# Optimization experiments

Measured on AMD Instinct MI355X. Metric: run time of the kernel, lower is better.

The kernel has to match this reference:

```python
import jax, jax.numpy as jnp
import numpy as np

N = 131072          # collocation points per dataset
C_WAVE = 1.0        # wave speed c
DIMS = [2, 256, 256, 256, 256, 1]


def _glorot(k, shape):
    fan_in, fan_out = shape
    std = jnp.sqrt(2.0 / (fan_in + fan_out)).astype(jnp.float32)
    return std * jax.random.normal(k, shape, dtype=jnp.float32)


def setup_inputs() -> dict:
    key = jax.random.key(0)
    ks = jax.random.split(key, 16)
    inp = {}
    for i in range(5):
        inp[f"W{i}"] = _glorot(ks[i], (DIMS[i], DIMS[i + 1]))
        inp[f"b{i}"] = jnp.zeros((DIMS[i + 1],), jnp.float32)
    inp["tx_equation"] = jax.random.uniform(ks[10], (N, 2), dtype=jnp.float32)
    inp["tx_init"] = jax.random.uniform(ks[11], (N, 2), dtype=jnp.float32)
    # initial condition points have t=0 in practice; values don't affect the math pattern
    inp["tx_init"] = inp["tx_init"].at[:, 0].set(0.0)
    inp["tx_bound"] = jax.random.uniform(ks[12], (N, 2), dtype=jnp.float32)
    return inp


def _mlp(params, tx):
    # tanh MLP: (..., 2) -> (..., 1)
    h = tx
    for W, b in params[:-1]:
        h = jnp.tanh(h @ W + b)
    W, b = params[-1]
    return h @ W + b


def reference(W0, b0, W1, b1, W2, b2, W3, b3, W4, b4,
              tx_equation, tx_init, tx_bound):
    params = [(W0, b0), (W1, b1), (W2, b2), (W3, b3), (W4, b4)]

    def u_scalar(tx):  # tx: (2,) -> scalar u(t, x)
        return _mlp(params, tx[None, :])[0, 0]

    # PDE residual: u_tt - c^2 * u_xx via per-point Hessian diagonal (input_diagonal_hessian)
    hess = jax.vmap(jax.hessian(u_scalar))(tx_equation)      # (N, 2, 2)
    u_tt = hess[:, 0, 0]
    u_xx = hess[:, 1, 1]
    pde_residual = (u_tt - (C_WAVE ** 2) * u_xx)[:, None]     # (N, 1)

    # Initial conditions: u and du/dt (input_gradient)
    u_init, g = jax.vmap(jax.value_and_grad(u_scalar))(tx_init)  # (N,), (N, 2)
    u_phi = u_init[:, None]                                   # (N, 1)
    du_dt_psi = g[:, 0][:, None]                              # (N, 1)

    # Boundary: plain forward
    u_bound = _mlp(params, tx_bound)                          # (N, 1)

    return jnp.stack([pde_residual, u_phi, du_dt_psi, u_bound], axis=0)  # (4, N, 1)
```

## Files before the change

kernel.cpp:

```cpp
#include <hip/hip_runtime.h>
#include <math.h>

#define N_PTS 131072
#define HID   256

typedef __attribute__((ext_vector_type(8)))  _Float16 f16x8;
typedef __attribute__((ext_vector_type(4)))  float    f32x4;
typedef __attribute__((ext_vector_type(16))) float    f32x16;
typedef unsigned int u32;
typedef __attribute__((address_space(1))) const u32 gu32;
typedef __attribute__((address_space(3))) u32       lu32;

#define LDS_ACT 0
#define LDS_B   32768
#define LDS_SZ  49152

__device__ __forceinline__ int act_addr(int row, int kbyte) {
    return row * 512 + ((kbyte + ((row & 31) << 4)) & 511);
}
__device__ __forceinline__ void tanh_f1(float z, float& h, float& f1) {
    float s = __expf(2.0f * z);
    float r = __builtin_amdgcn_rcpf(s + 1.0f);
    h  = fmaf(-2.0f, r, 1.0f);
    f1 = (1.0f - h) * (1.0f + h);
}

__global__ void prep_w(const float* __restrict__ W1, const float* __restrict__ W2,
                       const float* __restrict__ W3, char* __restrict__ ws)
{
    int idx = blockIdx.x * 256 + threadIdx.x;
    int l = idx >> 16;
    int e = idx & 65535;
    int k = e >> 8, n = e & 255;
    const float* W = (l == 0) ? W1 : (l == 1) ? W2 : W3;
    float w = W[e];
    int kc = k >> 4, hh = (k >> 3) & 1, kl = k & 7;
    int wq = n >> 5, nn = n & 31;
    size_t base = (size_t)((l * 16 + kc) * 8 + wq) * 1024;
    int byte_in = hh * 512 + nn * 16 + kl * 2;
    *(_Float16*)(ws + base + byte_in) = (_Float16)w;
}

template<int S, int PTS>
__global__ void __launch_bounds__(512, 4)
pinn_mfma(const float* __restrict__ W0, const float* __restrict__ b0,
          const float* __restrict__ b1, const float* __restrict__ b2,
          const float* __restrict__ b3,
          const float* __restrict__ W4, const float* __restrict__ b4,
          const char* __restrict__ wpre,
          const float* __restrict__ tx, float* __restrict__ out)
{
    extern __shared__ char lds[];
    const int tid  = threadIdx.x;
    const int lane = tid & 63;
    const int wid  = tid >> 6;
    const int l31  = lane & 31;
    const int hh   = lane >> 5;
    const int h16  = hh << 4;
    const int pbase = blockIdx.x * PTS;
    constexpr int CG = 512 / PTS;
    constexpr int NC = 256 / CG;
    const int ep  = tid / CG;
    const int ec0 = (tid % CG) * NC;

    {
        const float tt = tx[2 * (pbase + ep) + 0];
        const float xx = tx[2 * (pbase + ep) + 1];
        for (int cb = ec0; cb < ec0 + NC; cb += 8) {
            alignas(16) float w0r[8], w1r[8], bb[8];
            *(f32x4*)&w0r[0] = *(const f32x4*)(W0 + cb);
            *(f32x4*)&w0r[4] = *(const f32x4*)(W0 + cb + 4);
            *(f32x4*)&w1r[0] = *(const f32x4*)(W0 + HID + cb);
            *(f32x4*)&w1r[4] = *(const f32x4*)(W0 + HID + cb + 4);
            *(f32x4*)&bb[0]  = *(const f32x4*)(b0 + cb);
            *(f32x4*)&bb[4]  = *(const f32x4*)(b0 + cb + 4);
            f16x8 vhi[S];
            #pragma unroll
            for (int j = 0; j < 8; ++j) {
                float z = fmaf(tt, w0r[j], fmaf(xx, w1r[j], bb[j]));
                float h, f1;
                tanh_f1(z, h, f1);
                vhi[0][j] = (_Float16)h;
                if (S == 2) {
                    vhi[1][j] = (_Float16)(f1 * w0r[j]);
                } else if (S == 4) {
                    float d1 = w0r[j] + w1r[j];
                    float d2 = w0r[j] - w1r[j];
                    float f2 = -2.0f * h * f1;
                    vhi[1][j] = (_Float16)(f1 * d1);
                    vhi[2][j] = (_Float16)(f1 * d2);
                    vhi[3][j] = (_Float16)(f2 * d1 * d2);
                }
            }
            #pragma unroll
            for (int s2 = 0; s2 < S; ++s2) {
                int row = ep * S + s2;
                *(f16x8*)(lds + LDS_ACT + act_addr(row, cb * 2)) = vhi[s2];
            }
        }
    }

    const int c0 = wid * 32 + l31;
    const float b1a = b1[c0];
    const float b2a = b2[c0];
    const float b3a = b3[c0];

    const char* srcW = wpre + (size_t)wid * 1024 + lane * 16;
    char* dstW = lds + LDS_B + wid * 2048 + lane * 16;

    __builtin_amdgcn_sched_barrier(0);
    __builtin_amdgcn_global_load_lds((gu32*)srcW, (lu32*)dstW, 16, 0, 0);
    asm volatile("s_waitcnt lgkmcnt(0)" ::: "memory");
    __builtin_amdgcn_sched_barrier(0);
    __builtin_amdgcn_s_barrier();
    __builtin_amdgcn_sched_barrier(0);

    for (int l = 0; l < 3; ++l) {
        const float bias = (l == 0) ? b1a : (l == 1) ? b2a : b3a;
        const char* srcL = srcW + (size_t)l * 131072;

        f32x16 acc0 = (f32x16){0.f,0.f,0.f,0.f,0.f,0.f,0.f,0.f,
                               0.f,0.f,0.f,0.f,0.f,0.f,0.f,0.f};
        f32x16 acc1 = acc0;

        #pragma unroll
        for (int ph = 0; ph < 16; ++ph) {
            asm volatile("s_waitcnt vmcnt(0)" ::: "memory");

            const char* bslab = lds + LDS_B + wid * 2048 + (ph & 1) * 1024 + hh * 512;
            const int kbyte = ph * 32 + h16;
            f16x8 av0 = *(const f16x8*)(lds + LDS_ACT + act_addr(l31,      kbyte));
            f16x8 av1 = *(const f16x8*)(lds + LDS_ACT + act_addr(32 + l31, kbyte));
            f16x8 bv  = *(const f16x8*)(bslab + l31 * 16);

            if (ph < 15 || l < 2) {
                __builtin_amdgcn_global_load_lds(
                    (gu32*)(srcL + (size_t)(ph + 1) * 8192),
                    (lu32*)(dstW + ((ph + 1) & 1) * 1024), 16, 0, 0);
            }

            __builtin_amdgcn_s_setprio(1);
            acc0 = __builtin_amdgcn_mfma_f32_32x32x16_f16(av0, bv, acc0, 0, 0, 0);
            acc1 = __builtin_amdgcn_mfma_f32_32x32x16_f16(av1, bv, acc1, 0, 0, 0);
            __builtin_amdgcn_s_setprio(0);
        }
        __builtin_amdgcn_s_barrier();

        const bool lastL = (l == 2);
        const int colj = wid * 32 + l31;
        #pragma unroll
        for (int i = 0; i < 2; ++i) {
            const f32x16& A = i ? acc1 : acc0;
            const int rtb = i * 32 + 4 * hh;
            #pragma unroll
            for (int q = 0; q < 4; ++q) {
                const int rb = rtb + 8 * q;
                if (S == 4) {
                    float z0 = A[4*q+0] + bias;
                    float z1 = A[4*q+1];
                    float z2 = A[4*q+2];
                    float zm = A[4*q+3];
                    float h, f1;
                    tanh_f1(z0, h, f1);
                    float f2 = -2.0f * h * f1;
                    if (!lastL) {
                        *(_Float16*)(lds + LDS_ACT + act_addr(rb+0, colj*2)) = (_Float16)h;
                        *(_Float16*)(lds + LDS_ACT + act_addr(rb+1, colj*2)) = (_Float16)(f1 * z1);
                        *(_Float16*)(lds + LDS_ACT + act_addr(rb+2, colj*2)) = (_Float16)(f1 * z2);
                    }
                    *(_Float16*)(lds + LDS_ACT + act_addr(rb+3, colj*2)) =
                        (_Float16)(fmaf(f1, zm, f2 * z1 * z2));
                } else if (S == 2) {
                    #pragma unroll
                    for (int pp = 0; pp < 2; ++pp) {
                        float z0 = A[4*q+2*pp+0] + bias;
                        float zd = A[4*q+2*pp+1];
                        float h, f1;
                        tanh_f1(z0, h, f1);
                        *(_Float16*)(lds + LDS_ACT + act_addr(rb+2*pp+0, colj*2)) = (_Float16)h;
                        *(_Float16*)(lds + LDS_ACT + act_addr(rb+2*pp+1, colj*2)) = (_Float16)(f1 * zd);
                    }
                } else {
                    #pragma unroll
                    for (int m = 0; m < 4; ++m) {
                        float z0 = A[4*q+m] + bias;
                        float h, f1;
                        tanh_f1(z0, h, f1);
                        *(_Float16*)(lds + LDS_ACT + act_addr(rb+m, colj*2)) = (_Float16)h;
                    }
                }
            }
        }
        asm volatile("s_waitcnt lgkmcnt(0)" ::: "memory");
        __builtin_amdgcn_sched_barrier(0);
        __builtin_amdgcn_s_barrier();
        __builtin_amdgcn_sched_barrier(0);
    }

    if (S == 4) {
        const int p   = tid >> 5;
        const int seg = tid & 31;
        const int k0  = seg * 8;
        const int row = 4 * p + 3;
        f16x8 h8 = *(const f16x8*)(lds + LDS_ACT + act_addr(row, k0 * 2));
        alignas(16) float wv[8];
        *(f32x4*)&wv[0] = *(const f32x4*)(W4 + k0);
        *(f32x4*)&wv[4] = *(const f32x4*)(W4 + k0 + 4);
        float d = 0.0f;
        #pragma unroll
        for (int j = 0; j < 8; ++j) d = fmaf((float)h8[j], wv[j], d);
        #pragma unroll
        for (int off = 16; off > 0; off >>= 1) d += __shfl_down(d, off, 32);
        if (seg == 0) out[0 * N_PTS + pbase + p] = d;
    } else {
        const int row = tid >> 3;
        const int seg = tid & 7;
        const int k0  = seg * 32;
        float d = 0.0f;
        #pragma unroll
        for (int kb = 0; kb < 32; kb += 8) {
            f16x8 h8 = *(const f16x8*)(lds + LDS_ACT + act_addr(row, (k0 + kb) * 2));
            alignas(16) float wv[8];
            *(f32x4*)&wv[0] = *(const f32x4*)(W4 + k0 + kb);
            *(f32x4*)&wv[4] = *(const f32x4*)(W4 + k0 + kb + 4);
            #pragma unroll
            for (int j = 0; j < 8; ++j) d = fmaf((float)h8[j], wv[j], d);
        }
        d += __shfl_down(d, 4, 8);
        d += __shfl_down(d, 2, 8);
        d += __shfl_down(d, 1, 8);
        if (seg == 0) {
            if (S == 2) {
                const int p = row >> 1;
                if ((row & 1) == 0) out[1 * N_PTS + pbase + p] = d + b4[0];
                else                out[2 * N_PTS + pbase + p] = d;
            } else {
                out[3 * N_PTS + pbase + row] = d + b4[0];
            }
        }
    }
}

extern "C" void kernel_launch(void* const* d_in, const int* in_sizes, int n_in,
                              void* d_out, int out_size, void* d_ws, size_t ws_size,
                              hipStream_t stream) {
    const float* W0 = (const float*)d_in[0];
    const float* b0 = (const float*)d_in[1];
    const float* W1 = (const float*)d_in[2];
    const float* b1 = (const float*)d_in[3];
    const float* W2 = (const float*)d_in[4];
    const float* b2 = (const float*)d_in[5];
    const float* W3 = (const float*)d_in[6];
    const float* b3 = (const float*)d_in[7];
    const float* W4 = (const float*)d_in[8];
    const float* b4 = (const float*)d_in[9];
    const float* tx_eq    = (const float*)d_in[10];
    const float* tx_init  = (const float*)d_in[11];
    const float* tx_bound = (const float*)d_in[12];
    float* out = (float*)d_out;
    char* wpre = (char*)d_ws;

    prep_w<<<768, 256, 0, stream>>>(W1, W2, W3, wpre);
    pinn_mfma<4,16><<<N_PTS/16, 512, LDS_SZ, stream>>>(W0,b0,b1,b2,b3,W4,b4,wpre,tx_eq,   out);
    pinn_mfma<2,32><<<N_PTS/32, 512, LDS_SZ, stream>>>(W0,b0,b1,b2,b3,W4,b4,wpre,tx_init, out);
    pinn_mfma<1,64><<<N_PTS/64, 512, LDS_SZ, stream>>>(W0,b0,b1,b2,b3,W4,b4,wpre,tx_bound,out);
}
```

Baseline: 578.8 us.

## Hold MLP weight fragments in registers instead of staging through LDS

Weight B-fragments for each hidden layer are now loaded from global memory into a 16-entry register array and fed straight to the MFMAs. The next layer's fragments are prefetched into the same registers right after each MFMA pair. The LDS double-buffer and its per-phase vmcnt waits are removed, and LDS shrinks to a static 32 KB activation buffer. The aim is fewer LDS reads and waits in the inner loop and a smaller LDS footprint, at the cost of 64 extra VGPRs per thread under the existing launch bounds of 512 threads and 4 blocks.

```diff
diff --git a/kernel.cpp b/kernel.cpp
--- a/kernel.cpp
+++ b/kernel.cpp
@@ -7,13 +7,6 @@
 typedef __attribute__((ext_vector_type(8)))  _Float16 f16x8;
 typedef __attribute__((ext_vector_type(4)))  float    f32x4;
 typedef __attribute__((ext_vector_type(16))) float    f32x16;
-typedef unsigned int u32;
-typedef __attribute__((address_space(1))) const u32 gu32;
-typedef __attribute__((address_space(3))) u32       lu32;
-
-#define LDS_ACT 0
-#define LDS_B   32768
-#define LDS_SZ  49152
 
 __device__ __forceinline__ int act_addr(int row, int kbyte) {
     return row * 512 + ((kbyte + ((row & 31) << 4)) & 511);
@@ -50,7 +43,7 @@
           const char* __restrict__ wpre,
           const float* __restrict__ tx, float* __restrict__ out)
 {
-    extern __shared__ char lds[];
+    __shared__ char act[32768];
     const int tid  = threadIdx.x;
     const int lane = tid & 63;
     const int wid  = tid >> 6;
@@ -62,6 +55,13 @@
     constexpr int NC = 256 / CG;
     const int ep  = tid / CG;
     const int ec0 = (tid % CG) * NC;
+
+    const char* srcW = wpre + (size_t)wid * 1024 + lane * 16;
+
+    f16x8 bw[16];
+    #pragma unroll
+    for (int ph = 0; ph < 16; ++ph)
+        bw[ph] = *(const f16x8*)(srcW + (size_t)ph * 8192);
 
     {
         const float tt = tx[2 * (pbase + ep) + 0];
@@ -95,7 +95,7 @@
             #pragma unroll
             for (int s2 = 0; s2 < S; ++s2) {
                 int row = ep * S + s2;
-                *(f16x8*)(lds + LDS_ACT + act_addr(row, cb * 2)) = vhi[s2];
+                *(f16x8*)(act + act_addr(row, cb * 2)) = vhi[s2];
             }
         }
     }
@@ -105,11 +105,6 @@
     const float b2a = b2[c0];
     const float b3a = b3[c0];
 
-    const char* srcW = wpre + (size_t)wid * 1024 + lane * 16;
-    char* dstW = lds + LDS_B + wid * 2048 + lane * 16;
-
-    __builtin_amdgcn_sched_barrier(0);
-    __builtin_amdgcn_global_load_lds((gu32*)srcW, (lu32*)dstW, 16, 0, 0);
     asm volatile("s_waitcnt lgkmcnt(0)" ::: "memory");
     __builtin_amdgcn_sched_barrier(0);
     __builtin_amdgcn_s_barrier();
@@ -117,7 +112,8 @@
 
     for (int l = 0; l < 3; ++l) {
         const float bias = (l == 0) ? b1a : (l == 1) ? b2a : b3a;
-        const char* srcL = srcW + (size_t)l * 131072;
+        const char* srcNext = srcW + (size_t)(l + 1) * 131072;
+        const bool reload = (l < 2);
 
         f32x16 acc0 = (f32x16){0.f,0.f,0.f,0.f,0.f,0.f,0.f,0.f,
                                0.f,0.f,0.f,0.f,0.f,0.f,0.f,0.f};
@@ -125,24 +121,17 @@
 
         #pragma unroll
         for (int ph = 0; ph < 16; ++ph) {
-            asm volatile("s_waitcnt vmcnt(0)" ::: "memory");
-
-            const char* bslab = lds + LDS_B + wid * 2048 + (ph & 1) * 1024 + hh * 512;
             const int kbyte = ph * 32 + h16;
-            f16x8 av0 = *(const f16x8*)(lds + LDS_ACT + act_addr(l31,      kbyte));
-            f16x8 av1 = *(const f16x8*)(lds + LDS_ACT + act_addr(32 + l31, kbyte));
-            f16x8 bv  = *(const f16x8*)(bslab + l31 * 16);
-
-            if (ph < 15 || l < 2) {
-                __builtin_amdgcn_global_load_lds(
-                    (gu32*)(srcL + (size_t)(ph + 1) * 8192),
-                    (lu32*)(dstW + ((ph + 1) & 1) * 1024), 16, 0, 0);
-            }
+            f16x8 av0 = *(const f16x8*)(act + act_addr(l31,      kbyte));
+            f16x8 av1 = *(const f16x8*)(act + act_addr(32 + l31, kbyte));
 
             __builtin_amdgcn_s_setprio(1);
-            acc0 = __builtin_amdgcn_mfma_f32_32x32x16_f16(av0, bv, acc0, 0, 0, 0);
-            acc1 = __builtin_amdgcn_mfma_f32_32x32x16_f16(av1, bv, acc1, 0, 0, 0);
+            acc0 = __builtin_amdgcn_mfma_f32_32x32x16_f16(av0, bw[ph], acc0, 0, 0, 0);
+            acc1 = __builtin_amdgcn_mfma_f32_32x32x16_f16(av1, bw[ph], acc1, 0, 0, 0);
             __builtin_amdgcn_s_setprio(0);
+
+            if (reload)
+                bw[ph] = *(const f16x8*)(srcNext + (size_t)ph * 8192);
         }
         __builtin_amdgcn_s_barrier();
 
@@ -164,11 +153,11 @@
                     tanh_f1(z0, h, f1);
                     float f2 = -2.0f * h * f1;
                     if (!lastL) {
-                        *(_Float16*)(lds + LDS_ACT + act_addr(rb+0, colj*2)) = (_Float16)h;
-                        *(_Float16*)(lds + LDS_ACT + act_addr(rb+1, colj*2)) = (_Float16)(f1 * z1);
-                        *(_Float16*)(lds + LDS_ACT + act_addr(rb+2, colj*2)) = (_Float16)(f1 * z2);
+                        *(_Float16*)(act + act_addr(rb+0, colj*2)) = (_Float16)h;
+                        *(_Float16*)(act + act_addr(rb+1, colj*2)) = (_Float16)(f1 * z1);
+                        *(_Float16*)(act + act_addr(rb+2, colj*2)) = (_Float16)(f1 * z2);
                     }
-                    *(_Float16*)(lds + LDS_ACT + act_addr(rb+3, colj*2)) =
+                    *(_Float16*)(act + act_addr(rb+3, colj*2)) =
                         (_Float16)(fmaf(f1, zm, f2 * z1 * z2));
                 } else if (S == 2) {
                     #pragma unroll
@@ -177,8 +166,8 @@
                         float zd = A[4*q+2*pp+1];
                         float h, f1;
                         tanh_f1(z0, h, f1);
-                        *(_Float16*)(lds + LDS_ACT + act_addr(rb+2*pp+0, colj*2)) = (_Float16)h;
-                        *(_Float16*)(lds + LDS_ACT + act_addr(rb+2*pp+1, colj*2)) = (_Float16)(f1 * zd);
+                        *(_Float16*)(act + act_addr(rb+2*pp+0, colj*2)) = (_Float16)h;
+                        *(_Float16*)(act + act_addr(rb+2*pp+1, colj*2)) = (_Float16)(f1 * zd);
                     }
                 } else {
                     #pragma unroll
@@ -186,7 +175,7 @@
                         float z0 = A[4*q+m] + bias;
                         float h, f1;
                         tanh_f1(z0, h, f1);
-                        *(_Float16*)(lds + LDS_ACT + act_addr(rb+m, colj*2)) = (_Float16)h;
+                        *(_Float16*)(act + act_addr(rb+m, colj*2)) = (_Float16)h;
                     }
                 }
             }
@@ -202,7 +191,7 @@
         const int seg = tid & 31;
         const int k0  = seg * 8;
         const int row = 4 * p + 3;
-        f16x8 h8 = *(const f16x8*)(lds + LDS_ACT + act_addr(row, k0 * 2));
+        f16x8 h8 = *(const f16x8*)(act + act_addr(row, k0 * 2));
         alignas(16) float wv[8];
         *(f32x4*)&wv[0] = *(const f32x4*)(W4 + k0);
         *(f32x4*)&wv[4] = *(const f32x4*)(W4 + k0 + 4);
@@ -219,7 +208,7 @@
         float d = 0.0f;
         #pragma unroll
         for (int kb = 0; kb < 32; kb += 8) {
-            f16x8 h8 = *(const f16x8*)(lds + LDS_ACT + act_addr(row, (k0 + kb) * 2));
+            f16x8 h8 = *(const f16x8*)(act + act_addr(row, (k0 + kb) * 2));
             alignas(16) float wv[8];
             *(f32x4*)&wv[0] = *(const f32x4*)(W4 + k0 + kb);
             *(f32x4*)&wv[4] = *(const f32x4*)(W4 + k0 + kb + 4);
@@ -261,7 +250,7 @@
     char* wpre = (char*)d_ws;
 
     prep_w<<<768, 256, 0, stream>>>(W1, W2, W3, wpre);
-    pinn_mfma<4,16><<<N_PTS/16, 512, LDS_SZ, stream>>>(W0,b0,b1,b2,b3,W4,b4,wpre,tx_eq,   out);
-    pinn_mfma<2,32><<<N_PTS/32, 512, LDS_SZ, stream>>>(W0,b0,b1,b2,b3,W4,b4,wpre,tx_init, out);
-    pinn_mfma<1,64><<<N_PTS/64, 512, LDS_SZ, stream>>>(W0,b0,b1,b2,b3,W4,b4,wpre,tx_bound,out);
-}
+    pinn_mfma<4,16><<<N_PTS/16, 512, 0, stream>>>(W0,b0,b1,b2,b3,W4,b4,wpre,tx_eq,   out);
+    pinn_mfma<2,32><<<N_PTS/32, 512, 0, stream>>>(W0,b0,b1,b2,b3,W4,b4,wpre,tx_init, out);
+    pinn_mfma<1,64><<<N_PTS/64, 512, 0, stream>>>(W0,b0,b1,b2,b3,W4,b4,wpre,tx_bound,out);
+}
```

Result: slower. 849.9 us (+46.8%).
